# Kernel optimization log

Measured on AMD Instinct MI355X. Metric: run time of the kernel, lower is better.

Reference implementation:

```python
import jax, jax.numpy as jnp
import numpy as np

B, N, E = 16, 2048, 1_048_576          # graphs, residues per graph, total edges
IN_C, DIM, OUT_C, ENC_H, N_ATOMS = 256, 128, 6, 100, 20
NT = B * N


def setup_inputs() -> dict:
    key = jax.random.key(0)
    ks = jax.random.split(key, 24)
    s = 0.02
    x_res = jax.random.normal(ks[0], (NT, IN_C), jnp.float32)
    coords = jax.random.normal(ks[1], (NT, 3), jnp.float32)
    batch = jnp.repeat(jnp.arange(B, dtype=jnp.int32), N)
    src = jax.random.randint(ks[2], (E,), 0, NT, dtype=jnp.int32)
    dst = (src // N) * N + jax.random.randint(ks[3], (E,), 0, N, dtype=jnp.int32)
    edge_index = jnp.stack([src, dst])  # intra-graph edges, global node ids
    return {
        'x_res': x_res, 'coords': coords,
        'edge_index': edge_index, 'batch': batch,
        'bn_gamma': jnp.ones((IN_C,), jnp.float32),
        'bn_beta': jnp.zeros((IN_C,), jnp.float32),
        'W1': s * jax.random.normal(ks[4], (IN_C, 2 * DIM), jnp.float32),
        'b1': jnp.zeros((2 * DIM,), jnp.float32),
        'W2': s * jax.random.normal(ks[5], (2 * DIM, DIM), jnp.float32),
        'b2': jnp.zeros((DIM,), jnp.float32),
        'W3': s * jax.random.normal(ks[6], (DIM, N_ATOMS), jnp.float32),
        'b3': jnp.zeros((N_ATOMS,), jnp.float32),
        'embed': s * jax.random.normal(ks[7], (N_ATOMS + 1, DIM), jnp.float32),
        'W_msg': s * jax.random.normal(ks[8], (DIM, DIM), jnp.float32),
        'b_msg': jnp.zeros((DIM,), jnp.float32),
        'w_coor': s * jax.random.normal(ks[9], (DIM, 3), jnp.float32),
        'A1': s * jax.random.normal(ks[10], (DIM, ENC_H), jnp.float32),
        'a1': jnp.zeros((ENC_H,), jnp.float32),
        'A2': s * jax.random.normal(ks[11], (ENC_H, OUT_C), jnp.float32),
        'a2': jnp.zeros((OUT_C,), jnp.float32),
        'dyt_alpha': jnp.float32(0.5),
        'dyt_w': jnp.ones((OUT_C,), jnp.float32),
        'dyt_b': jnp.zeros((OUT_C,), jnp.float32),
    }


def reference(x_res, coords, edge_index, batch,
              bn_gamma, bn_beta, W1, b1, W2, b2, W3, b3,
              embed, W_msg, b_msg, w_coor,
              A1, a1, A2, a2, dyt_alpha, dyt_w, dyt_b):
    gelu = lambda v: jax.nn.gelu(v, approximate=False)
    # BatchNorm1d (train-mode batch stats, biased var, eps=1e-5); dropout is identity in eval
    mu = x_res.mean(0)
    var = x_res.var(0)
    xn = (x_res - mu) / jnp.sqrt(var + 1e-5) * bn_gamma + bn_beta
    # input2atomids MLP -> argmax atom ids
    h1 = gelu(xn @ W1 + b1)
    h2 = gelu(h1 @ W2 + b2)
    logits = h2 @ W3 + b3
    ids = jnp.argmax(logits, axis=-1)          # [NT]
    ids_b = ids.reshape(B, N)                  # equal-sized graphs -> no padding needed
    coords_b = coords.reshape(B, N, 3)
    # vectorized edge-list -> dense per-graph adjacency scatter
    g = batch[edge_index[0]]                   # graph id per edge
    ls = edge_index[0] - g * N                 # local src index
    ld = edge_index[1] - g * N                 # local dst index
    same = batch[edge_index[1]] == g           # keep intra-graph edges only
    adj = jnp.zeros((B, N, N), jnp.bool_).at[g, ls, ld].max(same)
    # GotenNet stand-in: embed atom ids, one adjacency-masked aggregation layer
    emb_ids = jnp.where(ids_b < 0, N_ATOMS, ids_b)   # -1 pad -> pad embedding row
    h = embed[emb_ids]                          # [B,N,DIM]
    adjf = adj.astype(h.dtype)
    deg = jnp.maximum(adjf.sum(-1, keepdims=True), 1.0)
    m = jnp.einsum('bij,bjd->bid', adjf, h) / deg
    hout = gelu((h + m) @ W_msg + b_msg)        # invariant features [B,N,DIM]
    coors_out = coords_b + jnp.tanh(hout @ w_coor)
    # un-pad / flatten back to node list, then out_angles head
    z = hout.reshape(NT, DIM)
    t = gelu(z @ A1 + a1)
    t = gelu(t @ A2 + a2)
    t = jnp.tanh(dyt_alpha * t) * dyt_w + dyt_b  # DynamicTanh (channels_last)
    angles = jnp.tanh(t)                         # [NT, OUT_C]
    return angles, z, coors_out
```

## Files before the change

kernel.cpp:

```cpp
#include <hip/hip_runtime.h>
#include <hip/hip_bf16.h>
#include <math.h>

#define Bg 16
#define Nn 2048
#define Ee (1<<20)
#define NT (Bg*Nn)
#define INC 256
#define DIMd 128
#define OUTC 6
#define ENCH 100
#define NATOMS 20

typedef __attribute__((ext_vector_type(8))) short bf16x8;
typedef __attribute__((ext_vector_type(4))) float f32x4;

__device__ __forceinline__ float gelu_f(float x){
    return 0.5f*x*(1.0f+erff(x*0.70710678118654752440f));
}
__device__ __forceinline__ unsigned short f2b(float f){
    __hip_bfloat16 h = __float2bfloat16(f);
    return *(unsigned short*)&h;
}
__device__ __forceinline__ float b2f(unsigned short u){
    unsigned v = ((unsigned)u)<<16;
    return __uint_as_float(v);
}
__device__ __forceinline__ void splitf(float v, unsigned short& hi, unsigned short& lo){
    unsigned short h = f2b(v);
    hi = h; lo = f2b(v - b2f(h));
}

__global__ __launch_bounds__(256) void bn_stats_k(const float* __restrict__ x,
                                                  float* __restrict__ stats){
    int c = threadIdx.x;
    int r0 = blockIdx.x * 128;
    const float* p = x + (size_t)r0*INC + c;
    float s = 0.f, s2 = 0.f;
    #pragma unroll 8
    for(int r=0;r<128;r++){ float v = p[(size_t)r*INC]; s += v; s2 += v*v; }
    atomicAdd(&stats[c], s);
    atomicAdd(&stats[INC+c], s2);
}

__global__ __launch_bounds__(256) void build_adj_k(const int* __restrict__ ei,
                                                   unsigned* __restrict__ mask){
    int e = blockIdx.x*256 + threadIdx.x;
    int s = ei[e], d = ei[Ee+e];
    if((s>>11) == (d>>11)){
        int ld = d & (Nn-1);
        atomicOr(&mask[(size_t)s*64 + (ld>>5)], 1u<<(ld&31));
    }
}

__global__ __launch_bounds__(256) void prep_w_k(const float* __restrict__ W1,
    const float* __restrict__ W2, const float* __restrict__ Wm,
    const float* __restrict__ A1, short* __restrict__ w1th, short* __restrict__ w1tl,
    short* __restrict__ w2th, short* __restrict__ w2tl,
    short* __restrict__ wmth, short* __restrict__ wmtl,
    short* __restrict__ a1th, short* __restrict__ a1tl)
{
    int gid = blockIdx.x*256 + threadIdx.x;
    unsigned short hi, lo;
    for(int l=gid;l<65536;l+=16384){ int n=l>>8,k=l&255;
        splitf(W1[(size_t)k*256+n],hi,lo); w1th[l]=(short)hi; w1tl[l]=(short)lo; }
    for(int l=gid;l<32768;l+=16384){ int n=l>>8,k=l&255;
        splitf(W2[(size_t)k*128+n],hi,lo); w2th[l]=(short)hi; w2tl[l]=(short)lo; }
    for(int l=gid;l<16384;l+=16384){ int n=l>>7,k=l&127;
        splitf(Wm[(size_t)k*128+n],hi,lo); wmth[l]=(short)hi; wmtl[l]=(short)lo; }
    for(int l=gid;l<16384;l+=16384){ int n=l>>7,k=l&127;
        float v=(n<ENCH)? A1[(size_t)k*ENCH+n] : 0.f;
        splitf(v,hi,lo); a1th[l]=(short)hi; a1tl[l]=(short)lo; }
}

__global__ __launch_bounds__(256) void gemm1_mfma(const float* __restrict__ x,
    const float* __restrict__ stats, const float* __restrict__ gamma,
    const float* __restrict__ beta, const short* __restrict__ w1th,
    const short* __restrict__ w1tl, const float* __restrict__ b1,
    float* __restrict__ h1)
{
    __shared__ float sc[256], sh[256];
    __shared__ short sAh[64*40], sAl[64*40];
    __shared__ short sBh[128*40], sBl[128*40];
    int tid = threadIdx.x;
    {
        float mu  = stats[tid]*(1.0f/NT);
        float var = stats[256+tid]*(1.0f/NT) - mu*mu;
        float s = gamma[tid]/sqrtf(var + 1e-5f);
        sc[tid] = s; sh[tid] = beta[tid] - mu*s;
    }
    int mb = blockIdx.x>>1, nb = blockIdx.x&1;
    int row0 = mb*64, n0 = nb*128;
    int lane = tid&63, w = tid>>6;
    int ln = lane&15, quad = lane>>4;
    int m0w = (w&1)*32, n0w = (w>>1)*64;
    f32x4 acc[2][4];
    #pragma unroll
    for(int i=0;i<2;i++)
        #pragma unroll
        for(int j=0;j<4;j++) acc[i][j] = (f32x4){0.f,0.f,0.f,0.f};
    __syncthreads();
    for(int k0=0;k0<256;k0+=32){
        #pragma unroll
        for(int i=0;i<2;i++){
            int id = tid + i*256; int r = id>>3, kq = (id&7)*4;
            float4 vx = *(const float4*)&x[(size_t)(row0+r)*256 + k0+kq];
            int k = k0+kq;
            float v0 = vx.x*sc[k]+sh[k],   v1 = vx.y*sc[k+1]+sh[k+1];
            float v2 = vx.z*sc[k+2]+sh[k+2], v3 = vx.w*sc[k+3]+sh[k+3];
            ushort4 hi, lo;
            splitf(v0,hi.x,lo.x); splitf(v1,hi.y,lo.y);
            splitf(v2,hi.z,lo.z); splitf(v3,hi.w,lo.w);
            *(ushort4*)&sAh[r*40+kq] = hi;
            *(ushort4*)&sAl[r*40+kq] = lo;
        }
        #pragma unroll
        for(int i=0;i<4;i++){
            int id = tid + i*256; int plane = id>>9, cid = id&511;
            int r = cid>>2, c = cid&3;
            const short* src = (plane? w1tl : w1th) + (size_t)(n0+r)*256 + k0 + c*8;
            short* dst = (plane? sBl : sBh) + r*40 + c*8;
            *(bf16x8*)dst = *(const bf16x8*)src;
        }
        __syncthreads();
        bf16x8 ah[2], al[2];
        #pragma unroll
        for(int tm=0;tm<2;tm++){
            ah[tm] = *(const bf16x8*)&sAh[(m0w+tm*16+ln)*40 + quad*8];
            al[tm] = *(const bf16x8*)&sAl[(m0w+tm*16+ln)*40 + quad*8];
        }
        #pragma unroll
        for(int tn=0;tn<4;tn++){
            bf16x8 bh = *(const bf16x8*)&sBh[(n0w+tn*16+ln)*40 + quad*8];
            bf16x8 bl = *(const bf16x8*)&sBl[(n0w+tn*16+ln)*40 + quad*8];
            #pragma unroll
            for(int tm=0;tm<2;tm++){
                acc[tm][tn] = __builtin_amdgcn_mfma_f32_16x16x32_bf16(al[tm], bh, acc[tm][tn], 0,0,0);
                acc[tm][tn] = __builtin_amdgcn_mfma_f32_16x16x32_bf16(ah[tm], bl, acc[tm][tn], 0,0,0);
                acc[tm][tn] = __builtin_amdgcn_mfma_f32_16x16x32_bf16(ah[tm], bh, acc[tm][tn], 0,0,0);
            }
        }
        __syncthreads();
    }
    #pragma unroll
    for(int tn=0;tn<4;tn++){
        int col = n0 + n0w + tn*16 + ln;
        float bias = b1[col];
        #pragma unroll
        for(int tm=0;tm<2;tm++){
            int rowb = row0 + m0w + tm*16 + quad*4;
            #pragma unroll
            for(int r=0;r<4;r++)
                h1[(size_t)(rowb+r)*256 + col] = gelu_f(acc[tm][tn][r] + bias);
        }
    }
}

__global__ __launch_bounds__(256) void gemm23_mfma(const float* __restrict__ h1,
    const short* __restrict__ w2th, const short* __restrict__ w2tl,
    const float* __restrict__ b2, const float* __restrict__ W3,
    const float* __restrict__ b3, int* __restrict__ ids)
{
    __shared__ short sAh[64*40], sAl[64*40];
    __shared__ short sBh[128*40], sBl[128*40];
    __shared__ float h2s[64*132];
    __shared__ float lgs[64*20];
    int tid = threadIdx.x;
    int row0 = blockIdx.x*64;
    int lane = tid&63, w = tid>>6;
    int ln = lane&15, quad = lane>>4;
    int m0w = (w&1)*32, n0w = (w>>1)*64;
    f32x4 acc[2][4];
    #pragma unroll
    for(int i=0;i<2;i++)
        #pragma unroll
        for(int j=0;j<4;j++) acc[i][j] = (f32x4){0.f,0.f,0.f,0.f};
    for(int k0=0;k0<256;k0+=32){
        #pragma unroll
        for(int i=0;i<2;i++){
            int id = tid + i*256; int r = id>>3, kq = (id&7)*4;
            float4 vx = *(const float4*)&h1[(size_t)(row0+r)*256 + k0+kq];
            ushort4 hi, lo;
            splitf(vx.x,hi.x,lo.x); splitf(vx.y,hi.y,lo.y);
            splitf(vx.z,hi.z,lo.z); splitf(vx.w,hi.w,lo.w);
            *(ushort4*)&sAh[r*40+kq] = hi;
            *(ushort4*)&sAl[r*40+kq] = lo;
        }
        #pragma unroll
        for(int i=0;i<4;i++){
            int id = tid + i*256; int plane = id>>9, cid = id&511;
            int r = cid>>2, c = cid&3;
            const short* src = (plane? w2tl : w2th) + (size_t)r*256 + k0 + c*8;
            short* dst = (plane? sBl : sBh) + r*40 + c*8;
            *(bf16x8*)dst = *(const bf16x8*)src;
        }
        __syncthreads();
        bf16x8 ah[2], al[2];
        #pragma unroll
        for(int tm=0;tm<2;tm++){
            ah[tm] = *(const bf16x8*)&sAh[(m0w+tm*16+ln)*40 + quad*8];
            al[tm] = *(const bf16x8*)&sAl[(m0w+tm*16+ln)*40 + quad*8];
        }
        #pragma unroll
        for(int tn=0;tn<4;tn++){
            bf16x8 bh = *(const bf16x8*)&sBh[(n0w+tn*16+ln)*40 + quad*8];
            bf16x8 bl = *(const bf16x8*)&sBl[(n0w+tn*16+ln)*40 + quad*8];
            #pragma unroll
            for(int tm=0;tm<2;tm++){
                acc[tm][tn] = __builtin_amdgcn_mfma_f32_16x16x32_bf16(al[tm], bh, acc[tm][tn], 0,0,0);
                acc[tm][tn] = __builtin_amdgcn_mfma_f32_16x16x32_bf16(ah[tm], bl, acc[tm][tn], 0,0,0);
                acc[tm][tn] = __builtin_amdgcn_mfma_f32_16x16x32_bf16(ah[tm], bh, acc[tm][tn], 0,0,0);
            }
        }
        __syncthreads();
    }
    #pragma unroll
    for(int tn=0;tn<4;tn++){
        int col = n0w + tn*16 + ln;
        float bias = b2[col];
        #pragma unroll
        for(int tm=0;tm<2;tm++){
            int rb = m0w + tm*16 + quad*4;
            #pragma unroll
            for(int r=0;r<4;r++)
                h2s[(rb+r)*132 + col] = gelu_f(acc[tm][tn][r] + bias);
        }
    }
    float* w3s = (float*)sBh;
    for(int l=tid;l<2560;l+=256) w3s[l] = W3[l];
    __syncthreads();
    int n = tid>>2, q = tid&3;
    float lg[5] = {};
    #pragma unroll 4
    for(int k=0;k<128;k++){
        float h = h2s[n*132+k];
        #pragma unroll
        for(int a=0;a<5;a++) lg[a] += h*w3s[k*20 + q*5 + a];
    }
    #pragma unroll
    for(int a=0;a<5;a++) lgs[n*20 + q*5 + a] = lg[a] + b3[q*5+a];
    __syncthreads();
    if(tid<64){
        float best = lgs[tid*20]; int bi = 0;
        #pragma unroll
        for(int a=1;a<20;a++){ float v2 = lgs[tid*20+a]; if(v2>best){best=v2;bi=a;} }
        ids[row0+tid] = bi;
    }
}

__global__ __launch_bounds__(256) void agg_k(const int* __restrict__ ids,
    const unsigned* __restrict__ mask, const float* __restrict__ embed,
    unsigned short* __restrict__ vbf)
{
    __shared__ unsigned ind[NATOMS*64];
    __shared__ unsigned char sid[2048];
    __shared__ float emb[NATOMS*128];
    int tid = threadIdx.x;
    int g = blockIdx.x>>5, tile = blockIdx.x&31;
    int lane = tid&63, wid = tid>>6;
    for(int l=tid;l<NATOMS*128;l+=256) emb[l] = embed[l];
    #pragma unroll
    for(int i=0;i<8;i++){ int j = tid + i*256; sid[j] = (unsigned char)ids[g*Nn + j]; }
    int node = tid>>2, p = tid&3;
    const unsigned* mrow = &mask[((size_t)(g*Nn + tile*64 + node))*64 + p*16];
    uint4 m0 = *(const uint4*)&mrow[0];
    uint4 m1 = *(const uint4*)&mrow[4];
    uint4 m2 = *(const uint4*)&mrow[8];
    uint4 m3 = *(const uint4*)&mrow[12];
    __syncthreads();
    for(int wp=wid; wp<32; wp+=4){
        int a = sid[wp*64 + lane];
        #pragma unroll
        for(int atom=0; atom<NATOMS; atom++){
            unsigned long long bm = __ballot(a==atom);
            if(lane<2) ind[atom*64 + wp*2 + lane] = (unsigned)(bm >> (32*lane));
        }
    }
    __syncthreads();
    unsigned mw[16];
    *(uint4*)&mw[0]=m0; *(uint4*)&mw[4]=m1; *(uint4*)&mw[8]=m2; *(uint4*)&mw[12]=m3;
    int degi = 0;
    #pragma unroll
    for(int w2=0;w2<16;w2++) degi += __popc(mw[w2]);
    float cnt[NATOMS];
    #pragma unroll
    for(int a=0;a<NATOMS;a++){
        int c = 0;
        const unsigned* ia = &ind[a*64 + p*16];
        #pragma unroll
        for(int w2=0;w2<16;w2++) c += __popc(mw[w2] & ia[w2]);
        cnt[a] = (float)c;
    }
    #pragma unroll
    for(int a=0;a<NATOMS;a++){
        cnt[a] += __shfl_xor(cnt[a],1,64);
        cnt[a] += __shfl_xor(cnt[a],2,64);
    }
    float deg = (float)degi;
    deg += __shfl_xor(deg,1,64);
    deg += __shfl_xor(deg,2,64);
    {
        float inv = 1.0f / fmaxf(deg, 1.0f);
        int oid = sid[tile*64 + node];
        int d0 = p*32;
        float vv[32];
        #pragma unroll
        for(int d=0;d<32;d++) vv[d]=0.f;
        #pragma unroll
        for(int a=0;a<NATOMS;a++){
            float ca = cnt[a];
            const float* ea = &emb[a*128 + d0];
            #pragma unroll
            for(int d=0;d<32;d+=4){
                float4 e = *(const float4*)&ea[d];
                vv[d]+=ca*e.x; vv[d+1]+=ca*e.y; vv[d+2]+=ca*e.z; vv[d+3]+=ca*e.w;
            }
        }
        const float* eo = &emb[oid*128 + d0];
        unsigned short* dst = &vbf[((size_t)(g*Nn + tile*64 + node))*128 + d0];
        #pragma unroll
        for(int d=0;d<32;d+=4){
            float4 e = *(const float4*)&eo[d];
            ushort4 o;
            o.x = f2b(e.x + vv[d]*inv);
            o.y = f2b(e.y + vv[d+1]*inv);
            o.z = f2b(e.z + vv[d+2]*inv);
            o.w = f2b(e.w + vv[d+3]*inv);
            *(ushort4*)&dst[d] = o;
        }
    }
}

__global__ __launch_bounds__(256) void msg2_k(
    const unsigned short* __restrict__ vbf,
    const short* __restrict__ wmth, const short* __restrict__ wmtl,
    const float* __restrict__ b_msg, const float* __restrict__ w_coor,
    const short* __restrict__ a1th, const short* __restrict__ a1tl,
    const float* __restrict__ a1v, const float* __restrict__ A2,
    const float* __restrict__ a2v, const float* __restrict__ dalpha,
    const float* __restrict__ dw, const float* __restrict__ db,
    const float* __restrict__ coords, float* __restrict__ out_ang,
    float* __restrict__ out_z, float* __restrict__ out_co)
{
    __shared__ short sA[64*40];
    __shared__ short sBh[128*40], sBl[128*40];
    __shared__ unsigned short houts[64*136];
    __shared__ float s_bm[128], s_wc[384], s_A2[624], s_a1[104];
    __shared__ float s_dyt[16], s_a2[8];
    int tid = threadIdx.x;
    int row0 = blockIdx.x*64;
    int lane = tid&63, w = tid>>6;
    int ln = lane&15, quad = lane>>4;
    int m0w = (w&1)*32, n0w = (w>>1)*64;

    if(tid<128) s_bm[tid] = b_msg[tid];
    if(tid<104) s_a1[tid] = (tid<ENCH) ? a1v[tid] : 0.f;
    for(int l=tid;l<384;l+=256) s_wc[l] = w_coor[l];
    for(int l=tid;l<624;l+=256) s_A2[l] = (l<600) ? A2[l] : 0.f;
    if(tid==0)  s_dyt[0] = dalpha[0];
    if(tid<6){ s_dyt[1+tid] = dw[tid]; s_dyt[8+tid] = db[tid]; }
    if(tid<8)  s_a2[tid] = (tid<6) ? a2v[tid] : 0.f;

    f32x4 acc[2][4];
    #pragma unroll
    for(int i=0;i<2;i++)
        #pragma unroll
        for(int j=0;j<4;j++) acc[i][j] = (f32x4){0.f,0.f,0.f,0.f};
    for(int k0=0;k0<128;k0+=32){
        {   int r = tid>>2, c = tid&3;
            *(bf16x8*)&sA[r*40+c*8] =
                *(const bf16x8*)&vbf[(size_t)(row0+r)*128 + k0 + c*8];
        }
        #pragma unroll
        for(int i=0;i<4;i++){
            int id = tid + i*256; int plane = id>>9, cid = id&511;
            int r = cid>>2, c = cid&3;
            const short* src = (plane? wmtl : wmth) + (size_t)r*128 + k0 + c*8;
            short* dst = (plane? sBl : sBh) + r*40 + c*8;
            *(bf16x8*)dst = *(const bf16x8*)src;
        }
        __syncthreads();
        bf16x8 av[2];
        #pragma unroll
        for(int tm=0;tm<2;tm++)
            av[tm] = *(const bf16x8*)&sA[(m0w+tm*16+ln)*40 + quad*8];
        #pragma unroll
        for(int tn=0;tn<4;tn++){
            bf16x8 bh = *(const bf16x8*)&sBh[(n0w+tn*16+ln)*40 + quad*8];
            bf16x8 bl = *(const bf16x8*)&sBl[(n0w+tn*16+ln)*40 + quad*8];
            #pragma unroll
            for(int tm=0;tm<2;tm++){
                acc[tm][tn] = __builtin_amdgcn_mfma_f32_16x16x32_bf16(av[tm], bl, acc[tm][tn], 0,0,0);
                acc[tm][tn] = __builtin_amdgcn_mfma_f32_16x16x32_bf16(av[tm], bh, acc[tm][tn], 0,0,0);
            }
        }
        __syncthreads();
    }
    #pragma unroll
    for(int tn=0;tn<4;tn++){
        int col = n0w + tn*16 + ln;
        float bias = s_bm[col];
        #pragma unroll
        for(int tm=0;tm<2;tm++){
            int mb2 = m0w + tm*16 + quad*4;
            #pragma unroll
            for(int r=0;r<4;r++){
                float hv = gelu_f(acc[tm][tn][r] + bias);
                out_z[(size_t)(row0+mb2+r)*128 + col] = hv;
                houts[(mb2+r)*136 + col] = f2b(hv);
            }
        }
    }
    __syncthreads();

    int node = tid>>2, p = tid&3;
    {
        float d0=0.f, d1=0.f, d2=0.f;
        int kb = p*32;
        #pragma unroll
        for(int k=0;k<32;k+=4){
            ushort4 hv = *(const ushort4*)&houts[node*136 + kb + k];
            float h0=b2f(hv.x),h1=b2f(hv.y),h2=b2f(hv.z),h3=b2f(hv.w);
            const float* wc = &s_wc[(kb+k)*3];
            d0 += h0*wc[0]+h1*wc[3]+h2*wc[6]+h3*wc[9];
            d1 += h0*wc[1]+h1*wc[4]+h2*wc[7]+h3*wc[10];
            d2 += h0*wc[2]+h1*wc[5]+h2*wc[8]+h3*wc[11];
        }
        d0 += __shfl_xor(d0,1,64); d0 += __shfl_xor(d0,2,64);
        d1 += __shfl_xor(d1,1,64); d1 += __shfl_xor(d1,2,64);
        d2 += __shfl_xor(d2,1,64); d2 += __shfl_xor(d2,2,64);
        if(p==0){
            size_t o = (size_t)(row0+node)*3;
            out_co[o+0] = coords[o+0] + tanhf(d0);
            out_co[o+1] = coords[o+1] + tanhf(d1);
            out_co[o+2] = coords[o+2] + tanhf(d2);
        }
    }

    f32x4 acc2[2][4];
    #pragma unroll
    for(int i=0;i<2;i++)
        #pragma unroll
        for(int j=0;j<4;j++) acc2[i][j] = (f32x4){0.f,0.f,0.f,0.f};
    for(int k0=0;k0<128;k0+=32){
        __syncthreads();
        #pragma unroll
        for(int i=0;i<4;i++){
            int id = tid + i*256; int plane = id>>9, cid = id&511;
            int r = cid>>2, c = cid&3;
            const short* src = (plane? a1tl : a1th) + (size_t)r*128 + k0 + c*8;
            short* dst = (plane? sBl : sBh) + r*40 + c*8;
            *(bf16x8*)dst = *(const bf16x8*)src;
        }
        __syncthreads();
        bf16x8 ah[2];
        #pragma unroll
        for(int tm=0;tm<2;tm++)
            ah[tm] = *(const bf16x8*)&houts[(m0w+tm*16+ln)*136 + k0 + quad*8];
        #pragma unroll
        for(int tn=0;tn<4;tn++){
            bf16x8 bh = *(const bf16x8*)&sBh[(n0w+tn*16+ln)*40 + quad*8];
            bf16x8 bl = *(const bf16x8*)&sBl[(n0w+tn*16+ln)*40 + quad*8];
            #pragma unroll
            for(int tm=0;tm<2;tm++){
                acc2[tm][tn] = __builtin_amdgcn_mfma_f32_16x16x32_bf16(ah[tm], bl, acc2[tm][tn], 0,0,0);
                acc2[tm][tn] = __builtin_amdgcn_mfma_f32_16x16x32_bf16(ah[tm], bh, acc2[tm][tn], 0,0,0);
            }
        }
    }
    __syncthreads();
    unsigned short* t1s = houts;
    #pragma unroll
    for(int tn=0;tn<4;tn++){
        int col = n0w + tn*16 + ln;
        if(col < 104){
            float bias = s_a1[col];
            #pragma unroll
            for(int tm=0;tm<2;tm++){
                int mb2 = m0w + tm*16 + quad*4;
                #pragma unroll
                for(int r=0;r<4;r++)
                    t1s[(mb2+r)*104 + col] = f2b(gelu_f(acc2[tm][tn][r] + bias));
            }
        }
    }
    __syncthreads();

    {
        int g0 = (p<2) ? p*7 : 14+(p-2)*6;
        int gcount = (p<2) ? 7 : 6;
        float s[6] = {0.f,0.f,0.f,0.f,0.f,0.f};
        for(int gg=0; gg<gcount; gg++){
            int kb = (g0+gg)*4;
            ushort4 tv = *(const ushort4*)&t1s[node*104 + kb];
            float u0=b2f(tv.x), u1=b2f(tv.y), u2=b2f(tv.z), u3=b2f(tv.w);
            #pragma unroll
            for(int j=0;j<6;j++)
                s[j] += u0*s_A2[kb*6+j] + u1*s_A2[(kb+1)*6+j]
                      + u2*s_A2[(kb+2)*6+j] + u3*s_A2[(kb+3)*6+j];
        }
        #pragma unroll
        for(int j=0;j<6;j++){ s[j]+=__shfl_xor(s[j],1,64); s[j]+=__shfl_xor(s[j],2,64); }
        if(p<2){
            size_t o = (size_t)(row0+node)*6 + p*3;
            #pragma unroll
            for(int jj=0;jj<3;jj++){
                int j = p*3+jj;
                float t2v = gelu_f(s[j] + s_a2[j]);
                float uu = tanhf(s_dyt[0]*t2v)*s_dyt[1+j] + s_dyt[8+j];
                out_ang[o+jj] = tanhf(uu);
            }
        }
    }
}

extern "C" void kernel_launch(void* const* d_in, const int* in_sizes, int n_in,
                              void* d_out, int out_size, void* d_ws, size_t ws_size,
                              hipStream_t stream) {
    const float* x      = (const float*)d_in[0];
    const float* coords = (const float*)d_in[1];
    const int*   ei     = (const int*)d_in[2];
    const float* gamma  = (const float*)d_in[4];
    const float* beta   = (const float*)d_in[5];
    const float* W1     = (const float*)d_in[6];
    const float* b1     = (const float*)d_in[7];
    const float* W2     = (const float*)d_in[8];
    const float* b2     = (const float*)d_in[9];
    const float* W3     = (const float*)d_in[10];
    const float* b3     = (const float*)d_in[11];
    const float* embed  = (const float*)d_in[12];
    const float* W_msg  = (const float*)d_in[13];
    const float* b_msg  = (const float*)d_in[14];
    const float* w_coor = (const float*)d_in[15];
    const float* A1     = (const float*)d_in[16];
    const float* a1v    = (const float*)d_in[17];
    const float* A2     = (const float*)d_in[18];
    const float* a2v    = (const float*)d_in[19];
    const float* dalpha = (const float*)d_in[20];
    const float* dw     = (const float*)d_in[21];
    const float* db     = (const float*)d_in[22];

    char* ws = (char*)d_ws;
    int*      ids   = (int*)ws;
    float*    stats = (float*)(ws + 131072);
    short*    w1th  = (short*)(ws + 262144);
    short*    w1tl  = w1th + 65536;
    short*    w2th  = w1tl + 65536;
    short*    w2tl  = w2th + 32768;
    short*    wmth  = w2tl + 32768;
    short*    wmtl  = wmth + 16384;
    short*    a1th  = wmtl + 16384;
    short*    a1tl  = a1th + 16384;
    unsigned* mask  = (unsigned*)(ws + (1<<20));
    float*    h1    = (float*)(ws + (size_t)10*1048576);
    unsigned short* vbf = (unsigned short*)(ws + (size_t)10*1048576);

    float* out_ang = (float*)d_out;
    float* out_z   = out_ang + (size_t)NT*OUTC;
    float* out_co  = out_z   + (size_t)NT*DIMd;

    hipMemsetAsync(stats, 0, 2*INC*sizeof(float), stream);
    hipMemsetAsync(mask, 0, (size_t)NT*64*sizeof(unsigned), stream);
    bn_stats_k<<<256, 256, 0, stream>>>(x, stats);
    build_adj_k<<<Ee/256, 256, 0, stream>>>(ei, mask);
    prep_w_k<<<64, 256, 0, stream>>>(W1, W2, W_msg, A1,
        w1th, w1tl, w2th, w2tl, wmth, wmtl, a1th, a1tl);
    gemm1_mfma<<<1024, 256, 0, stream>>>(x, stats, gamma, beta, w1th, w1tl, b1, h1);
    gemm23_mfma<<<512, 256, 0, stream>>>(h1, w2th, w2tl, b2, W3, b3, ids);
    agg_k<<<512, 256, 0, stream>>>(ids, mask, embed, vbf);
    msg2_k<<<512, 256, 0, stream>>>(vbf, wmth, wmtl, b_msg, w_coor,
        a1th, a1tl, a1v, A2, a2v, dalpha, dw, db, coords, out_ang, out_z, out_co);
}
```

Baseline: 271.9 us.

## Fuse pipeline kernels: merge prep, gemm1+adjacency, agg+message; store h1 as bf16 split

Merges BN stats and weight prep into one launch. Folds the adjacency bitmask build into gemm1, which now computes all 256 columns per 64-row block. Fuses the neighbor aggregation into the message kernel so the aggregated features stay in shared memory instead of going through a global buffer. h1 is now stored as pre-split bf16 hi/lo planes, so gemm23 no longer re-splits fp32 values. The aim is fewer launches and less global traffic, at the cost of more shared memory and registers per block (8 accumulator tiles in gemm1), which may lower occupancy.

```diff
diff --git a/kernel.cpp b/kernel.cpp
--- a/kernel.cpp
+++ b/kernel.cpp
@@ -31,57 +31,49 @@
     hi = h; lo = f2b(v - b2f(h));
 }
 
-__global__ __launch_bounds__(256) void bn_stats_k(const float* __restrict__ x,
-                                                  float* __restrict__ stats){
-    int c = threadIdx.x;
-    int r0 = blockIdx.x * 128;
-    const float* p = x + (size_t)r0*INC + c;
-    float s = 0.f, s2 = 0.f;
-    #pragma unroll 8
-    for(int r=0;r<128;r++){ float v = p[(size_t)r*INC]; s += v; s2 += v*v; }
-    atomicAdd(&stats[c], s);
-    atomicAdd(&stats[INC+c], s2);
-}
-
-__global__ __launch_bounds__(256) void build_adj_k(const int* __restrict__ ei,
-                                                   unsigned* __restrict__ mask){
-    int e = blockIdx.x*256 + threadIdx.x;
-    int s = ei[e], d = ei[Ee+e];
-    if((s>>11) == (d>>11)){
-        int ld = d & (Nn-1);
-        atomicOr(&mask[(size_t)s*64 + (ld>>5)], 1u<<(ld&31));
-    }
-}
-
-__global__ __launch_bounds__(256) void prep_w_k(const float* __restrict__ W1,
+__global__ __launch_bounds__(256) void prep0_k(const float* __restrict__ x,
+    float* __restrict__ stats, const float* __restrict__ W1,
     const float* __restrict__ W2, const float* __restrict__ Wm,
     const float* __restrict__ A1, short* __restrict__ w1th, short* __restrict__ w1tl,
     short* __restrict__ w2th, short* __restrict__ w2tl,
     short* __restrict__ wmth, short* __restrict__ wmtl,
     short* __restrict__ a1th, short* __restrict__ a1tl)
 {
-    int gid = blockIdx.x*256 + threadIdx.x;
-    unsigned short hi, lo;
-    for(int l=gid;l<65536;l+=16384){ int n=l>>8,k=l&255;
-        splitf(W1[(size_t)k*256+n],hi,lo); w1th[l]=(short)hi; w1tl[l]=(short)lo; }
-    for(int l=gid;l<32768;l+=16384){ int n=l>>8,k=l&255;
-        splitf(W2[(size_t)k*128+n],hi,lo); w2th[l]=(short)hi; w2tl[l]=(short)lo; }
-    for(int l=gid;l<16384;l+=16384){ int n=l>>7,k=l&127;
-        splitf(Wm[(size_t)k*128+n],hi,lo); wmth[l]=(short)hi; wmtl[l]=(short)lo; }
-    for(int l=gid;l<16384;l+=16384){ int n=l>>7,k=l&127;
-        float v=(n<ENCH)? A1[(size_t)k*ENCH+n] : 0.f;
-        splitf(v,hi,lo); a1th[l]=(short)hi; a1tl[l]=(short)lo; }
-}
-
-__global__ __launch_bounds__(256) void gemm1_mfma(const float* __restrict__ x,
+    int bx = blockIdx.x, tid = threadIdx.x;
+    if(bx < 256){
+        int c = tid;
+        int r0 = bx * 128;
+        const float* p = x + (size_t)r0*INC + c;
+        float s = 0.f, s2 = 0.f;
+        #pragma unroll 8
+        for(int r=0;r<128;r++){ float v = p[(size_t)r*INC]; s += v; s2 += v*v; }
+        atomicAdd(&stats[c], s);
+        atomicAdd(&stats[INC+c], s2);
+    } else {
+        int gid = (bx-256)*256 + tid;
+        unsigned short hi, lo;
+        for(int l=gid;l<65536;l+=16384){ int n=l>>8,k=l&255;
+            splitf(W1[(size_t)k*256+n],hi,lo); w1th[l]=(short)hi; w1tl[l]=(short)lo; }
+        for(int l=gid;l<32768;l+=16384){ int n=l>>8,k=l&255;
+            splitf(W2[(size_t)k*128+n],hi,lo); w2th[l]=(short)hi; w2tl[l]=(short)lo; }
+        for(int l=gid;l<16384;l+=16384){ int n=l>>7,k=l&127;
+            splitf(Wm[(size_t)k*128+n],hi,lo); wmth[l]=(short)hi; wmtl[l]=(short)lo; }
+        for(int l=gid;l<16384;l+=16384){ int n=l>>7,k=l&127;
+            float v=(n<ENCH)? A1[(size_t)k*ENCH+n] : 0.f;
+            splitf(v,hi,lo); a1th[l]=(short)hi; a1tl[l]=(short)lo; }
+    }
+}
+
+__global__ __launch_bounds__(256) void gemm1_adj_k(const float* __restrict__ x,
     const float* __restrict__ stats, const float* __restrict__ gamma,
     const float* __restrict__ beta, const short* __restrict__ w1th,
     const short* __restrict__ w1tl, const float* __restrict__ b1,
-    float* __restrict__ h1)
+    unsigned short* __restrict__ h1h, unsigned short* __restrict__ h1l,
+    const int* __restrict__ ei, unsigned* __restrict__ mask)
 {
     __shared__ float sc[256], sh[256];
     __shared__ short sAh[64*40], sAl[64*40];
-    __shared__ short sBh[128*40], sBl[128*40];
+    __shared__ short sBh[256*40], sBl[256*40];
     int tid = threadIdx.x;
     {
         float mu  = stats[tid]*(1.0f/NT);
@@ -89,16 +81,15 @@
         float s = gamma[tid]/sqrtf(var + 1e-5f);
         sc[tid] = s; sh[tid] = beta[tid] - mu*s;
     }
-    int mb = blockIdx.x>>1, nb = blockIdx.x&1;
-    int row0 = mb*64, n0 = nb*128;
+    int row0 = blockIdx.x*64;
     int lane = tid&63, w = tid>>6;
     int ln = lane&15, quad = lane>>4;
-    int m0w = (w&1)*32, n0w = (w>>1)*64;
-    f32x4 acc[2][4];
+    int m0w = (w&1)*32, n0b = (w>>1)*128;
+    f32x4 acc[2][8];
     #pragma unroll
     for(int i=0;i<2;i++)
         #pragma unroll
-        for(int j=0;j<4;j++) acc[i][j] = (f32x4){0.f,0.f,0.f,0.f};
+        for(int j=0;j<8;j++) acc[i][j] = (f32x4){0.f,0.f,0.f,0.f};
     __syncthreads();
     for(int k0=0;k0<256;k0+=32){
         #pragma unroll
@@ -115,10 +106,10 @@
             *(ushort4*)&sAl[r*40+kq] = lo;
         }
         #pragma unroll
-        for(int i=0;i<4;i++){
-            int id = tid + i*256; int plane = id>>9, cid = id&511;
+        for(int i=0;i<8;i++){
+            int id = tid + i*256; int plane = id>>10, cid = id&1023;
             int r = cid>>2, c = cid&3;
-            const short* src = (plane? w1tl : w1th) + (size_t)(n0+r)*256 + k0 + c*8;
+            const short* src = (plane? w1tl : w1th) + (size_t)r*256 + k0 + c*8;
             short* dst = (plane? sBl : sBh) + r*40 + c*8;
             *(bf16x8*)dst = *(const bf16x8*)src;
         }
@@ -130,9 +121,9 @@
             al[tm] = *(const bf16x8*)&sAl[(m0w+tm*16+ln)*40 + quad*8];
         }
         #pragma unroll
-        for(int tn=0;tn<4;tn++){
-            bf16x8 bh = *(const bf16x8*)&sBh[(n0w+tn*16+ln)*40 + quad*8];
-            bf16x8 bl = *(const bf16x8*)&sBl[(n0w+tn*16+ln)*40 + quad*8];
+        for(int tn=0;tn<8;tn++){
+            bf16x8 bh = *(const bf16x8*)&sBh[(n0b+tn*16+ln)*40 + quad*8];
+            bf16x8 bl = *(const bf16x8*)&sBl[(n0b+tn*16+ln)*40 + quad*8];
             #pragma unroll
             for(int tm=0;tm<2;tm++){
                 acc[tm][tn] = __builtin_amdgcn_mfma_f32_16x16x32_bf16(al[tm], bh, acc[tm][tn], 0,0,0);
@@ -143,20 +134,36 @@
         __syncthreads();
     }
     #pragma unroll
-    for(int tn=0;tn<4;tn++){
-        int col = n0 + n0w + tn*16 + ln;
+    for(int tn=0;tn<8;tn++){
+        int col = n0b + tn*16 + ln;
         float bias = b1[col];
         #pragma unroll
         for(int tm=0;tm<2;tm++){
             int rowb = row0 + m0w + tm*16 + quad*4;
             #pragma unroll
-            for(int r=0;r<4;r++)
-                h1[(size_t)(rowb+r)*256 + col] = gelu_f(acc[tm][tn][r] + bias);
-        }
-    }
-}
-
-__global__ __launch_bounds__(256) void gemm23_mfma(const float* __restrict__ h1,
+            for(int r=0;r<4;r++){
+                float hv = gelu_f(acc[tm][tn][r] + bias);
+                unsigned short hi, lo;
+                splitf(hv, hi, lo);
+                h1h[(size_t)(rowb+r)*256 + col] = hi;
+                h1l[(size_t)(rowb+r)*256 + col] = lo;
+            }
+        }
+    }
+    int ebase = blockIdx.x*2048;
+    #pragma unroll
+    for(int i=0;i<8;i++){
+        int e = ebase + i*256 + tid;
+        int s = ei[e], d = ei[Ee+e];
+        if((s>>11) == (d>>11)){
+            int ld = d & (Nn-1);
+            atomicOr(&mask[(size_t)s*64 + (ld>>5)], 1u<<(ld&31));
+        }
+    }
+}
+
+__global__ __launch_bounds__(256) void gemm23_mfma(
+    const unsigned short* __restrict__ h1h, const unsigned short* __restrict__ h1l,
     const short* __restrict__ w2th, const short* __restrict__ w2tl,
     const float* __restrict__ b2, const float* __restrict__ W3,
     const float* __restrict__ b3, int* __restrict__ ids)
@@ -178,13 +185,12 @@
     for(int k0=0;k0<256;k0+=32){
         #pragma unroll
         for(int i=0;i<2;i++){
-            int id = tid + i*256; int r = id>>3, kq = (id&7)*4;
-            float4 vx = *(const float4*)&h1[(size_t)(row0+r)*256 + k0+kq];
-            ushort4 hi, lo;
-            splitf(vx.x,hi.x,lo.x); splitf(vx.y,hi.y,lo.y);
-            splitf(vx.z,hi.z,lo.z); splitf(vx.w,hi.w,lo.w);
-            *(ushort4*)&sAh[r*40+kq] = hi;
-            *(ushort4*)&sAl[r*40+kq] = lo;
+            int id = tid + i*256; int plane = id>>8, cid = id&255;
+            int r = cid>>2, c = cid&3;
+            const unsigned short* src = (plane? h1l : h1h)
+                                        + (size_t)(row0+r)*256 + k0 + c*8;
+            short* dst = (plane? sAl : sAh) + r*40 + c*8;
+            *(bf16x8*)dst = *(const bf16x8*)src;
         }
         #pragma unroll
         for(int i=0;i<4;i++){
@@ -248,91 +254,9 @@
     }
 }
 
-__global__ __launch_bounds__(256) void agg_k(const int* __restrict__ ids,
-    const unsigned* __restrict__ mask, const float* __restrict__ embed,
-    unsigned short* __restrict__ vbf)
-{
-    __shared__ unsigned ind[NATOMS*64];
-    __shared__ unsigned char sid[2048];
-    __shared__ float emb[NATOMS*128];
-    int tid = threadIdx.x;
-    int g = blockIdx.x>>5, tile = blockIdx.x&31;
-    int lane = tid&63, wid = tid>>6;
-    for(int l=tid;l<NATOMS*128;l+=256) emb[l] = embed[l];
-    #pragma unroll
-    for(int i=0;i<8;i++){ int j = tid + i*256; sid[j] = (unsigned char)ids[g*Nn + j]; }
-    int node = tid>>2, p = tid&3;
-    const unsigned* mrow = &mask[((size_t)(g*Nn + tile*64 + node))*64 + p*16];
-    uint4 m0 = *(const uint4*)&mrow[0];
-    uint4 m1 = *(const uint4*)&mrow[4];
-    uint4 m2 = *(const uint4*)&mrow[8];
-    uint4 m3 = *(const uint4*)&mrow[12];
-    __syncthreads();
-    for(int wp=wid; wp<32; wp+=4){
-        int a = sid[wp*64 + lane];
-        #pragma unroll
-        for(int atom=0; atom<NATOMS; atom++){
-            unsigned long long bm = __ballot(a==atom);
-            if(lane<2) ind[atom*64 + wp*2 + lane] = (unsigned)(bm >> (32*lane));
-        }
-    }
-    __syncthreads();
-    unsigned mw[16];
-    *(uint4*)&mw[0]=m0; *(uint4*)&mw[4]=m1; *(uint4*)&mw[8]=m2; *(uint4*)&mw[12]=m3;
-    int degi = 0;
-    #pragma unroll
-    for(int w2=0;w2<16;w2++) degi += __popc(mw[w2]);
-    float cnt[NATOMS];
-    #pragma unroll
-    for(int a=0;a<NATOMS;a++){
-        int c = 0;
-        const unsigned* ia = &ind[a*64 + p*16];
-        #pragma unroll
-        for(int w2=0;w2<16;w2++) c += __popc(mw[w2] & ia[w2]);
-        cnt[a] = (float)c;
-    }
-    #pragma unroll
-    for(int a=0;a<NATOMS;a++){
-        cnt[a] += __shfl_xor(cnt[a],1,64);
-        cnt[a] += __shfl_xor(cnt[a],2,64);
-    }
-    float deg = (float)degi;
-    deg += __shfl_xor(deg,1,64);
-    deg += __shfl_xor(deg,2,64);
-    {
-        float inv = 1.0f / fmaxf(deg, 1.0f);
-        int oid = sid[tile*64 + node];
-        int d0 = p*32;
-        float vv[32];
-        #pragma unroll
-        for(int d=0;d<32;d++) vv[d]=0.f;
-        #pragma unroll
-        for(int a=0;a<NATOMS;a++){
-            float ca = cnt[a];
-            const float* ea = &emb[a*128 + d0];
-            #pragma unroll
-            for(int d=0;d<32;d+=4){
-                float4 e = *(const float4*)&ea[d];
-                vv[d]+=ca*e.x; vv[d+1]+=ca*e.y; vv[d+2]+=ca*e.z; vv[d+3]+=ca*e.w;
-            }
-        }
-        const float* eo = &emb[oid*128 + d0];
-        unsigned short* dst = &vbf[((size_t)(g*Nn + tile*64 + node))*128 + d0];
-        #pragma unroll
-        for(int d=0;d<32;d+=4){
-            float4 e = *(const float4*)&eo[d];
-            ushort4 o;
-            o.x = f2b(e.x + vv[d]*inv);
-            o.y = f2b(e.y + vv[d+1]*inv);
-            o.z = f2b(e.z + vv[d+2]*inv);
-            o.w = f2b(e.w + vv[d+3]*inv);
-            *(ushort4*)&dst[d] = o;
-        }
-    }
-}
-
-__global__ __launch_bounds__(256) void msg2_k(
-    const unsigned short* __restrict__ vbf,
+__global__ __launch_bounds__(256) void msg3_k(
+    const int* __restrict__ ids, const unsigned* __restrict__ mask,
+    const float* __restrict__ embed,
     const short* __restrict__ wmth, const short* __restrict__ wmtl,
     const float* __restrict__ b_msg, const float* __restrict__ w_coor,
     const short* __restrict__ a1th, const short* __restrict__ a1tl,
@@ -342,17 +266,28 @@
     const float* __restrict__ coords, float* __restrict__ out_ang,
     float* __restrict__ out_z, float* __restrict__ out_co)
 {
-    __shared__ short sA[64*40];
-    __shared__ short sBh[128*40], sBl[128*40];
+    __shared__ unsigned short v_bf[64*136];
     __shared__ unsigned short houts[64*136];
+    __shared__ __align__(16) unsigned char arena[20480];
     __shared__ float s_bm[128], s_wc[384], s_A2[624], s_a1[104];
     __shared__ float s_dyt[16], s_a2[8];
+
+    unsigned*       ind = (unsigned*)arena;
+    unsigned char*  sid = arena + 5120;
+    float*          emb = (float*)(arena + 7168);
+    short*          sBh = (short*)arena;
+    short*          sBl = (short*)(arena + 10240);
+
     int tid = threadIdx.x;
     int row0 = blockIdx.x*64;
+    int g = blockIdx.x>>5, tile = blockIdx.x&31;
     int lane = tid&63, w = tid>>6;
     int ln = lane&15, quad = lane>>4;
     int m0w = (w&1)*32, n0w = (w>>1)*64;
 
+    for(int l=tid;l<NATOMS*128;l+=256) emb[l] = embed[l];
+    #pragma unroll
+    for(int i=0;i<8;i++){ int j = tid + i*256; sid[j] = (unsigned char)ids[g*Nn + j]; }
     if(tid<128) s_bm[tid] = b_msg[tid];
     if(tid<104) s_a1[tid] = (tid<ENCH) ? a1v[tid] : 0.f;
     for(int l=tid;l<384;l+=256) s_wc[l] = w_coor[l];
@@ -361,16 +296,85 @@
     if(tid<6){ s_dyt[1+tid] = dw[tid]; s_dyt[8+tid] = db[tid]; }
     if(tid<8)  s_a2[tid] = (tid<6) ? a2v[tid] : 0.f;
 
+    int node = tid>>2, p = tid&3;
+    const unsigned* mrow = &mask[((size_t)(row0 + node))*64 + p*16];
+    uint4 mm0 = *(const uint4*)&mrow[0];
+    uint4 mm1 = *(const uint4*)&mrow[4];
+    uint4 mm2 = *(const uint4*)&mrow[8];
+    uint4 mm3 = *(const uint4*)&mrow[12];
+    __syncthreads();
+
+    for(int wp=w; wp<32; wp+=4){
+        int a = sid[wp*64 + lane];
+        #pragma unroll
+        for(int atom=0; atom<NATOMS; atom++){
+            unsigned long long bm = __ballot(a==atom);
+            if(lane<2) ind[atom*64 + wp*2 + lane] = (unsigned)(bm >> (32*lane));
+        }
+    }
+    __syncthreads();
+
+    unsigned mw[16];
+    *(uint4*)&mw[0]=mm0; *(uint4*)&mw[4]=mm1; *(uint4*)&mw[8]=mm2; *(uint4*)&mw[12]=mm3;
+    int degi = 0;
+    #pragma unroll
+    for(int w2=0;w2<16;w2++) degi += __popc(mw[w2]);
+    float cnt[NATOMS];
+    #pragma unroll
+    for(int a=0;a<NATOMS;a++){
+        int c = 0;
+        const unsigned* ia = &ind[a*64 + p*16];
+        #pragma unroll
+        for(int w2=0;w2<16;w2++) c += __popc(mw[w2] & ia[w2]);
+        cnt[a] = (float)c;
+    }
+    #pragma unroll
+    for(int a=0;a<NATOMS;a++){
+        cnt[a] += __shfl_xor(cnt[a],1,64);
+        cnt[a] += __shfl_xor(cnt[a],2,64);
+    }
+    float deg = (float)degi;
+    deg += __shfl_xor(deg,1,64);
+    deg += __shfl_xor(deg,2,64);
+
+    {
+        float inv = 1.0f / fmaxf(deg, 1.0f);
+        int oid = sid[tile*64 + node];
+        int d0 = p*32;
+        float vv[32];
+        #pragma unroll
+        for(int d=0;d<32;d++) vv[d]=0.f;
+        #pragma unroll
+        for(int a=0;a<NATOMS;a++){
+            float ca = cnt[a];
+            const float* ea = &emb[a*128 + d0];
+            #pragma unroll
+            for(int d=0;d<32;d+=4){
+                float4 e = *(const float4*)&ea[d];
+                vv[d]+=ca*e.x; vv[d+1]+=ca*e.y; vv[d+2]+=ca*e.z; vv[d+3]+=ca*e.w;
+            }
+        }
+        const float* eo = &emb[oid*128 + d0];
+        unsigned short* dst = &v_bf[node*136 + d0];
+        #pragma unroll
+        for(int d=0;d<32;d+=4){
+            float4 e = *(const float4*)&eo[d];
+            ushort4 o;
+            o.x = f2b(e.x + vv[d]*inv);
+            o.y = f2b(e.y + vv[d+1]*inv);
+            o.z = f2b(e.z + vv[d+2]*inv);
+            o.w = f2b(e.w + vv[d+3]*inv);
+            *(ushort4*)&dst[d] = o;
+        }
+    }
+    __syncthreads();
+
     f32x4 acc[2][4];
     #pragma unroll
     for(int i=0;i<2;i++)
         #pragma unroll
         for(int j=0;j<4;j++) acc[i][j] = (f32x4){0.f,0.f,0.f,0.f};
     for(int k0=0;k0<128;k0+=32){
-        {   int r = tid>>2, c = tid&3;
-            *(bf16x8*)&sA[r*40+c*8] =
-                *(const bf16x8*)&vbf[(size_t)(row0+r)*128 + k0 + c*8];
-        }
         #pragma unroll
         for(int i=0;i<4;i++){
             int id = tid + i*256; int plane = id>>9, cid = id&511;
@@ -383,7 +387,7 @@
         bf16x8 av[2];
         #pragma unroll
         for(int tm=0;tm<2;tm++)
-            av[tm] = *(const bf16x8*)&sA[(m0w+tm*16+ln)*40 + quad*8];
+            av[tm] = *(const bf16x8*)&v_bf[(m0w+tm*16+ln)*136 + k0 + quad*8];
         #pragma unroll
         for(int tn=0;tn<4;tn++){
             bf16x8 bh = *(const bf16x8*)&sBh[(n0w+tn*16+ln)*40 + quad*8];
@@ -413,7 +417,6 @@
     }
     __syncthreads();
 
-    int node = tid>>2, p = tid&3;
     {
         float d0=0.f, d1=0.f, d2=0.f;
         int kb = p*32;
@@ -552,8 +555,8 @@
     short*    a1th  = wmtl + 16384;
     short*    a1tl  = a1th + 16384;
     unsigned* mask  = (unsigned*)(ws + (1<<20));
-    float*    h1    = (float*)(ws + (size_t)10*1048576);
-    unsigned short* vbf = (unsigned short*)(ws + (size_t)10*1048576);
+    unsigned short* h1h = (unsigned short*)(ws + (size_t)10*1048576);
+    unsigned short* h1l = (unsigned short*)(ws + (size_t)27*1048576);
 
     float* out_ang = (float*)d_out;
     float* out_z   = out_ang + (size_t)NT*OUTC;
@@ -561,13 +564,11 @@
 
     hipMemsetAsync(stats, 0, 2*INC*sizeof(float), stream);
     hipMemsetAsync(mask, 0, (size_t)NT*64*sizeof(unsigned), stream);
-    bn_stats_k<<<256, 256, 0, stream>>>(x, stats);
-    build_adj_k<<<Ee/256, 256, 0, stream>>>(ei, mask);
-    prep_w_k<<<64, 256, 0, stream>>>(W1, W2, W_msg, A1,
+    prep0_k<<<320, 256, 0, stream>>>(x, stats, W1, W2, W_msg, A1,
         w1th, w1tl, w2th, w2tl, wmth, wmtl, a1th, a1tl);
-    gemm1_mfma<<<1024, 256, 0, stream>>>(x, stats, gamma, beta, w1th, w1tl, b1, h1);
-    gemm23_mfma<<<512, 256, 0, stream>>>(h1, w2th, w2tl, b2, W3, b3, ids);
-    agg_k<<<512, 256, 0, stream>>>(ids, mask, embed, vbf);
-    msg2_k<<<512, 256, 0, stream>>>(vbf, wmth, wmtl, b_msg, w_coor,
+    gemm1_adj_k<<<512, 256, 0, stream>>>(x, stats, gamma, beta, w1th, w1tl, b1,
+        h1h, h1l, ei, mask);
+    gemm23_mfma<<<512, 256, 0, stream>>>(h1h, h1l, w2th, w2tl, b2, W3, b3, ids);
+    msg3_k<<<512, 256, 0, stream>>>(ids, mask, embed, wmth, wmtl, b_msg, w_coor,
         a1th, a1tl, a1v, A2, a2v, dalpha, dw, db, coords, out_ang, out_z, out_co);
 }
```

After: 271.9 us. About the same (+0.0%).
